# Performance work log

Hardware: AMD Instinct MI355X
Metric: run time of the kernel (lower is better)

Reference implementation:

```python
import jax, jax.numpy as jnp
import numpy as np

DIM = 1024
HID = 2048
E = 8
K = 2
INV_SQRT2 = 1.0 / 1.41421356237


def setup_inputs() -> dict:
    key = jax.random.key(0)
    ks = jax.random.split(key, 10)
    s = lambda fan_in: 1.0 / np.sqrt(fan_in)
    return {
        "x": jax.random.normal(ks[0], (4, 2048, DIM), dtype=jnp.float32),
        "gate_w": jax.random.uniform(ks[1], (DIM, E), jnp.float32, -s(DIM), s(DIM)),
        "gate_b": jnp.zeros((E,), jnp.float32),
        "w1": jax.random.uniform(ks[2], (E, DIM, HID), jnp.float32, -s(DIM), s(DIM)),
        "b1": jnp.zeros((E, HID), jnp.float32),
        "w2": jax.random.uniform(ks[3], (E, DIM, HID), jnp.float32, -s(DIM), s(DIM)),
        "b2": jnp.zeros((E, HID), jnp.float32),
        "w3": jax.random.uniform(ks[4], (E, HID, DIM), jnp.float32, -s(HID), s(HID)),
        "b3": jnp.zeros((E, DIM), jnp.float32),
    }


def reference(x, gate_w, gate_b, w1, b1, w2, b2, w3, b3):
    # Gating
    logits = jnp.einsum("bsd,de->bse", x, gate_w) + gate_b          # [b,s,E]
    scores = jax.nn.softmax(logits, axis=-1)
    topk_scores, topk_idx = jax.lax.top_k(scores, K)                  # [b,s,K]

    # Load-balance (entropy) loss over mean expert usage
    usage = scores.mean(axis=(0, 1))                                   # [E]
    lb_loss = -(usage * jnp.log(usage + 1e-9)).sum()

    # Per-token combine weight for each expert: score if expert in top-k else 0
    onehot = jax.nn.one_hot(topk_idx, E, dtype=x.dtype)               # [b,s,K,E]
    comb = (topk_scores[..., None] * onehot).sum(axis=2)              # [b,s,E]

    # SwiGLU experts (batched over E via einsum)
    h = jnp.einsum("bsd,edh->ebsh", x, w1) + b1[:, None, None, :]
    g = jax.nn.silu(jnp.einsum("bsd,edh->ebsh", x, w2) + b2[:, None, None, :])
    eo = jnp.einsum("ebsh,ehd->ebsd", h * g, w3) + b3[:, None, None, :]
    eo = eo * INV_SQRT2

    # Weighted combine (zero weight where expert not selected)
    out = jnp.einsum("ebsd,bse->bsd", eo, comb)
    return out, lb_loss
```

## Files before the change

kernel.cpp:

```cpp
#include <hip/hip_runtime.h>
#include <cstdio>

#define NTOK 8192
#define DIM 1024
#define HID 2048
#define NE 8
#define NPAIR (NTOK * 2)

typedef __attribute__((ext_vector_type(8))) short bf16x8;
typedef __attribute__((ext_vector_type(4))) float f32x4;

typedef const __attribute__((address_space(1))) void* gas_ptr;
typedef __attribute__((address_space(3))) void* las_ptr;

__device__ __forceinline__ void async16(const void* g, void* s) {
  __builtin_amdgcn_global_load_lds((gas_ptr)g, (las_ptr)s, 16, 0, 0);
}

__device__ __forceinline__ unsigned short f2bf(float f) {
  unsigned int u = __float_as_uint(f);
  u = (u + 0x7fff + ((u >> 16) & 1)) >> 16;
  return (unsigned short)u;
}

__device__ __forceinline__ float bf2f(unsigned short u) {
  return __uint_as_float((unsigned int)u << 16);
}


#define S_BARRIER __builtin_amdgcn_s_barrier()
#define VM_WAIT(N) asm volatile("s_waitcnt vmcnt(" #N ")" ::: "memory")
#define LGKM0 asm volatile("s_waitcnt lgkmcnt(0)" ::: "memory")
#define CFENCE asm volatile("" ::: "memory")

__global__ __launch_bounds__(256) void prep_kernel(
    const float* __restrict__ w1, const float* __restrict__ w2,
    const float* __restrict__ w3, unsigned short* __restrict__ w1bt,
    unsigned short* __restrict__ w2bt, unsigned short* __restrict__ w3bt) {
  const int z = blockIdx.y;
  const int m = z >> 3, e = z & 7;
  int R, C;
  const float* in;
  unsigned short* outp;
  if (m == 0)      { R = DIM; C = HID; in = w1; outp = w1bt; }
  else if (m == 1) { R = DIM; C = HID; in = w2; outp = w2bt; }
  else             { R = HID; C = DIM; in = w3; outp = w3bt; }
  in += (size_t)e * DIM * HID;
  outp += (size_t)e * DIM * HID;

  const int tilesx = C >> 6;
  const int c0 = (blockIdx.x % tilesx) * 64;
  const int r0 = (blockIdx.x / tilesx) * 64;

  __shared__ float tT[64][65];
  const int tid = threadIdx.x;
  const int cq = tid & 15;
  const int rr = tid >> 4;

#pragma unroll
  for (int p = 0; p < 4; p++) {
    const int r = rr + p * 16;
    const float4 v = *(const float4*)(in + (size_t)(r0 + r) * C + c0 + cq * 4);
    tT[cq * 4 + 0][r] = v.x;
    tT[cq * 4 + 1][r] = v.y;
    tT[cq * 4 + 2][r] = v.z;
    tT[cq * 4 + 3][r] = v.w;
  }
  __syncthreads();
#pragma unroll
  for (int p = 0; p < 4; p++) {
    const int cc = rr + p * 16;
    ushort4 o;
    o.x = f2bf(tT[cc][cq * 4 + 0]);
    o.y = f2bf(tT[cc][cq * 4 + 1]);
    o.z = f2bf(tT[cc][cq * 4 + 2]);
    o.w = f2bf(tT[cc][cq * 4 + 3]);
    *(ushort4*)(outp + (size_t)(c0 + cc) * R + r0 + cq * 4) = o;
  }
}

__global__ __launch_bounds__(256) void gate_kernel(
    const float* __restrict__ x, const float* __restrict__ gw,
    const float* __restrict__ gb, unsigned short* __restrict__ xb,
    float* __restrict__ scores, int* __restrict__ route_e,
    float* __restrict__ route_w) {
  __shared__ float sgwT[NE][DIM];
  const int tid = threadIdx.x;
#pragma unroll
  for (int i = 0; i < 8; i++) {
    const int j = i * 256 + tid;
    const float4 v = ((const float4*)gw)[j];
    const int d = j >> 1, e0 = (j & 1) * 4;
    sgwT[e0 + 0][d] = v.x; sgwT[e0 + 1][d] = v.y;
    sgwT[e0 + 2][d] = v.z; sgwT[e0 + 3][d] = v.w;
  }
  __syncthreads();

  const int wv = tid >> 6, lane = tid & 63;
  const int t = blockIdx.x * 4 + wv;
  float acc[NE] = {0.f, 0.f, 0.f, 0.f, 0.f, 0.f, 0.f, 0.f};
  const float4* x4 = (const float4*)(x + (size_t)t * DIM);
#pragma unroll
  for (int i = 0; i < 4; i++) {
    const float4 xv = x4[i * 64 + lane];
    const int d4 = i * 64 + lane;
    ushort4 xbv;
    xbv.x = f2bf(xv.x); xbv.y = f2bf(xv.y);
    xbv.z = f2bf(xv.z); xbv.w = f2bf(xv.w);
    *(ushort4*)(xb + (size_t)t * DIM + d4 * 4) = xbv;
#pragma unroll
    for (int e = 0; e < NE; e++) {
      const float4 wv4 = *(const float4*)&sgwT[e][d4 * 4];
      acc[e] += xv.x * wv4.x + xv.y * wv4.y + xv.z * wv4.z + xv.w * wv4.w;
    }
  }
#pragma unroll
  for (int e = 0; e < NE; e++)
#pragma unroll
    for (int s = 32; s; s >>= 1) acc[e] += __shfl_xor(acc[e], s, 64);

  if (lane == 0) {
    float l[NE], m = -1e30f;
#pragma unroll
    for (int e = 0; e < NE; e++) { l[e] = acc[e] + gb[e]; m = fmaxf(m, l[e]); }
    float p[NE], sum = 0.f;
#pragma unroll
    for (int e = 0; e < NE; e++) { p[e] = __expf(l[e] - m); sum += p[e]; }
    const float inv = 1.f / sum;
    float s[NE];
#pragma unroll
    for (int e = 0; e < NE; e++) { s[e] = p[e] * inv; scores[t * NE + e] = s[e]; }
    int i1 = 0;
    for (int e = 1; e < NE; e++) if (s[e] > s[i1]) i1 = e;
    int i2 = -1;
    for (int e = 0; e < NE; e++) {
      if (e == i1) continue;
      if (i2 < 0 || s[e] > s[i2]) i2 = e;
    }
    route_e[t * 2] = i1; route_e[t * 2 + 1] = i2;
    route_w[t * 2] = s[i1]; route_w[t * 2 + 1] = s[i2];
  }
}

__global__ void finalize_kernel(const float* __restrict__ scores,
                                const int* __restrict__ route_e,
                                int* __restrict__ ctrl,
                                float* __restrict__ out_lb) {
  __shared__ float red[1024];
  __shared__ int hist[NE];
  const int tid = threadIdx.x;
  if (tid < NE) hist[tid] = 0;
  const int e = tid & 7, row = tid >> 3;
  float s = 0.f;
  for (int i = 0; i < 64; i++) s += scores[(size_t)(row + i * 128) * NE + e];
  red[tid] = s;
  __syncthreads();
#pragma unroll
  for (int i = 0; i < 16; i++)
    atomicAdd(&hist[route_e[i * 1024 + tid]], 1);
  for (int st = 512; st >= 8; st >>= 1) {
    __syncthreads();
    if (tid < st) red[tid] += red[tid + st];
  }
  __syncthreads();
  if (tid == 0) {
    float lb = 0.f;
    for (int ee = 0; ee < NE; ee++) {
      const float u = red[ee] * (1.f / 8192.f);
      lb -= u * __logf(u + 1e-9f);
    }
    *out_lb = lb;
    int o = 0;
    for (int ee = 0; ee < NE; ee++) {
      ctrl[ee] = hist[ee];
      ctrl[8 + ee] = o;
      ctrl[17 + ee] = o;
      o += hist[ee];
    }
    ctrl[16] = o;
  }
}

__global__ __launch_bounds__(256) void scatter_kernel(
    const int* __restrict__ route_e, const float* __restrict__ route_w,
    int* __restrict__ ctrl, int* __restrict__ tok_list,
    float* __restrict__ pair_w, int* __restrict__ pair_pos) {
  __shared__ int lh[NE];
  __shared__ int lbase[NE];
  const int tid = threadIdx.x;
  const int t = blockIdx.x * 256 + tid;
  if (tid < NE) lh[tid] = 0;
  __syncthreads();
  const int e0 = route_e[t * 2], e1 = route_e[t * 2 + 1];
  const int p0 = atomicAdd(&lh[e0], 1);
  const int p1 = atomicAdd(&lh[e1], 1);
  __syncthreads();
  if (tid < NE) lbase[tid] = atomicAdd(&ctrl[17 + tid], lh[tid]);
  __syncthreads();
  const int q0 = lbase[e0] + p0;
  const int q1 = lbase[e1] + p1;
  tok_list[q0] = t;
  pair_w[q0] = route_w[t * 2] * 0.70710678118654752f;
  pair_pos[t * 2] = q0;
  tok_list[q1] = t;
  pair_w[q1] = route_w[t * 2 + 1] * 0.70710678118654752f;
  pair_pos[t * 2 + 1] = q1;
}

__global__ __launch_bounds__(512) void stage1_kernel(
    const unsigned short* __restrict__ xb, const unsigned short* __restrict__ w1bt,
    const unsigned short* __restrict__ w2bt, const float* __restrict__ b1,
    const float* __restrict__ b2, const int* __restrict__ tok_list,
    const int* __restrict__ ctrl, unsigned short* __restrict__ act) {
  const int hbid = blockIdx.x;
  const int lid = ((hbid & 7) << 9) + (hbid >> 3);
  const int e = lid >> 9;
  const int ytile = (lid >> 4) & 31;
  const int h0 = (lid & 15) * 128;

  const int cnt = ctrl[e];
  if (ytile * 256 >= cnt) return;
  const int off = ctrl[8 + e];
  const int rows = min(256, cnt - ytile * 256);

  __shared__ unsigned short sX[4][256 * 32];
  __shared__ unsigned short sW1[4][128 * 32];
  __shared__ unsigned short sW2[4][128 * 32];

  const int tid = threadIdx.x;
  const int wv = tid >> 6, lane = tid & 63;

  const int cl = ((tid & 3) ^ ((tid >> 3) & 3)) * 8;

  const unsigned short* w1p = w1bt + (size_t)e * HID * DIM + (size_t)h0 * DIM;
  const unsigned short* w2p = w2bt + (size_t)e * HID * DIM + (size_t)h0 * DIM;
  const unsigned short* gx0 =
      xb + (size_t)tok_list[off + ytile * 256 + min(tid >> 2, rows - 1)] * DIM + cl;
  const unsigned short* gx1 =
      xb + (size_t)tok_list[off + ytile * 256 + min(128 + (tid >> 2), rows - 1)] * DIM + cl;
  const unsigned short* gw1 = w1p + (size_t)(tid >> 2) * DIM + cl;
  const unsigned short* gw2 = w2p + (size_t)(tid >> 2) * DIM + cl;

  f32x4 ah[8][2], ag[8][2];
#pragma unroll
  for (int i = 0; i < 8; i++)
#pragma unroll
    for (int j = 0; j < 2; j++) {
      ah[i][j] = (f32x4){0.f, 0.f, 0.f, 0.f};
      ag[i][j] = (f32x4){0.f, 0.f, 0.f, 0.f};
    }

  const int wr = wv >> 2, wc = wv & 3;
  const int l15 = lane & 15, q = lane >> 4;
  const int pch = (q ^ ((l15 >> 1) & 3)) * 8;

#define S1_STAGE(B)                                   \
  do {                                                \
    async16(gx0, sX[B] + (wv * 64) * 8);              \
    async16(gx1, sX[B] + (512 + wv * 64) * 8);        \
    async16(gw1, sW1[B] + (wv * 64) * 8);             \
    async16(gw2, sW2[B] + (wv * 64) * 8);             \
    gx0 += 32; gx1 += 32; gw1 += 32; gw2 += 32;       \
  } while (0)

  S1_STAGE(0); S1_STAGE(1); S1_STAGE(2);
  VM_WAIT(8);
  S_BARRIER;
  CFENCE;

  const int NT = DIM / 32;
  for (int t = 0; t < NT; t++) {
    const int cur = t & 3;
    bf16x8 bx[8], a1[2], a2[2];
    {
      const unsigned short* xs = sX[cur];
      const unsigned short* w1s = sW1[cur];
      const unsigned short* w2s = sW2[cur];
#pragma unroll
      for (int i = 0; i < 8; i++)
        bx[i] = *(const bf16x8*)(xs + (wr * 128 + i * 16 + l15) * 32 + pch);
#pragma unroll
      for (int j = 0; j < 2; j++) {
        a1[j] = *(const bf16x8*)(w1s + (wc * 32 + j * 16 + l15) * 32 + pch);
        a2[j] = *(const bf16x8*)(w2s + (wc * 32 + j * 16 + l15) * 32 + pch);
      }
    }
    if (t < NT - 3) {
      const int nb = (t + 3) & 3;
      S1_STAGE(nb);
    }
    S_BARRIER;
    LGKM0;
    __builtin_amdgcn_sched_barrier(0);
    __builtin_amdgcn_s_setprio(1);
#pragma unroll
    for (int i = 0; i < 8; i++) {
      ah[i][0] = __builtin_amdgcn_mfma_f32_16x16x32_bf16(a1[0], bx[i], ah[i][0], 0, 0, 0);
      ag[i][0] = __builtin_amdgcn_mfma_f32_16x16x32_bf16(a2[0], bx[i], ag[i][0], 0, 0, 0);
      ah[i][1] = __builtin_amdgcn_mfma_f32_16x16x32_bf16(a1[1], bx[i], ah[i][1], 0, 0, 0);
      ag[i][1] = __builtin_amdgcn_mfma_f32_16x16x32_bf16(a2[1], bx[i], ag[i][1], 0, 0, 0);
    }
    __builtin_amdgcn_s_setprio(0);
    if (t < NT - 3) VM_WAIT(8);
    else if (t == NT - 3) VM_WAIT(4);
    else if (t == NT - 2) VM_WAIT(0);
    CFENCE;
    S_BARRIER;
  }
#undef S1_STAGE

  f32x4 b1v[2], b2v[2];
#pragma unroll
  for (int j = 0; j < 2; j++) {
    const int hc = h0 + wc * 32 + j * 16 + q * 4;
    b1v[j] = *(const f32x4*)(b1 + e * HID + hc);
    b2v[j] = *(const f32x4*)(b2 + e * HID + hc);
  }
#pragma unroll
  for (int i = 0; i < 8; i++) {
    const int trow = wr * 128 + i * 16 + l15;
    if (trow < rows) {
      const size_t gp = (size_t)(off + ytile * 256 + trow) * HID;
#pragma unroll
      for (int j = 0; j < 2; j++) {
        const int hc = h0 + wc * 32 + j * 16 + q * 4;
        ushort4 o;
        {
          const float hh = ah[i][j][0] + b1v[j][0];
          const float gg = ag[i][j][0] + b2v[j][0];
          o.x = f2bf(hh * (gg / (1.f + __expf(-gg))));
        }
        {
          const float hh = ah[i][j][1] + b1v[j][1];
          const float gg = ag[i][j][1] + b2v[j][1];
          o.y = f2bf(hh * (gg / (1.f + __expf(-gg))));
        }
        {
          const float hh = ah[i][j][2] + b1v[j][2];
          const float gg = ag[i][j][2] + b2v[j][2];
          o.z = f2bf(hh * (gg / (1.f + __expf(-gg))));
        }
        {
          const float hh = ah[i][j][3] + b1v[j][3];
          const float gg = ag[i][j][3] + b2v[j][3];
          o.w = f2bf(hh * (gg / (1.f + __expf(-gg))));
        }
        *(ushort4*)(act + gp + hc) = o;
      }
    }
  }
}

__global__ __launch_bounds__(512) void stage2s_kernel(
    const unsigned short* __restrict__ act, const unsigned short* __restrict__ w3bt,
    const float* __restrict__ b3, const float* __restrict__ pair_w,
    const int* __restrict__ ctrl, unsigned short* __restrict__ pair_out) {
  const int hbid = blockIdx.x;
  const int lid = ((hbid & 7) << 7) + (hbid >> 3);
  const int e = lid >> 7;
  const int ytile = (lid >> 2) & 31;
  const int d0 = (lid & 3) * 256;

  const int cnt = ctrl[e];
  if (ytile * 256 >= cnt) return;
  const int off = ctrl[8 + e];
  const int rows = min(256, cnt - ytile * 256);
  const int rbase = off + ytile * 256;

  __shared__ unsigned short sA[4][256 * 32];
  __shared__ unsigned short sW[4][256 * 32];

  const int tid = threadIdx.x;
  const int wv = tid >> 6, lane = tid & 63;
  const int cl = ((tid & 3) ^ ((tid >> 3) & 3)) * 8;

  const unsigned short* w3p = w3bt + (size_t)e * DIM * HID + (size_t)d0 * HID;
  const unsigned short* ga0 =
      act + (size_t)(rbase + min(tid >> 2, rows - 1)) * HID + cl;
  const unsigned short* ga1 =
      act + (size_t)(rbase + min(128 + (tid >> 2), rows - 1)) * HID + cl;
  const unsigned short* gw0 = w3p + (size_t)(tid >> 2) * HID + cl;
  const unsigned short* gw1 = w3p + (size_t)(128 + (tid >> 2)) * HID + cl;

  f32x4 acc[8][4];
#pragma unroll
  for (int i = 0; i < 8; i++)
#pragma unroll
    for (int j = 0; j < 4; j++) acc[i][j] = (f32x4){0.f, 0.f, 0.f, 0.f};

  const int wr = wv >> 2, wc = wv & 3;
  const int l15 = lane & 15, q = lane >> 4;
  const int pch = (q ^ ((l15 >> 1) & 3)) * 8;

#define S2_STAGE(B)                                   \
  do {                                                \
    async16(ga0, sA[B] + (wv * 64) * 8);              \
    async16(ga1, sA[B] + (512 + wv * 64) * 8);        \
    async16(gw0, sW[B] + (wv * 64) * 8);              \
    async16(gw1, sW[B] + (512 + wv * 64) * 8);        \
    ga0 += 32; ga1 += 32; gw0 += 32; gw1 += 32;       \
  } while (0)

  S2_STAGE(0); S2_STAGE(1); S2_STAGE(2);
  VM_WAIT(8);
  S_BARRIER;
  CFENCE;

  const int NT = HID / 32;
  for (int t = 0; t < NT; t++) {
    const int cur = t & 3;
    bf16x8 af[8], bf[4];
    {
      const unsigned short* as = sA[cur];
      const unsigned short* ws = sW[cur];
#pragma unroll
      for (int i = 0; i < 8; i++)
        af[i] = *(const bf16x8*)(as + (wr * 128 + i * 16 + l15) * 32 + pch);
#pragma unroll
      for (int j = 0; j < 4; j++)
        bf[j] = *(const bf16x8*)(ws + (wc * 64 + j * 16 + l15) * 32 + pch);
    }
    if (t < NT - 3) {
      const int nb = (t + 3) & 3;
      S2_STAGE(nb);
    }
    S_BARRIER;
    LGKM0;
    __builtin_amdgcn_sched_barrier(0);
    __builtin_amdgcn_s_setprio(1);
#pragma unroll
    for (int i = 0; i < 8; i++)
#pragma unroll
      for (int j = 0; j < 4; j++)
        acc[i][j] =
            __builtin_amdgcn_mfma_f32_16x16x32_bf16(af[i], bf[j], acc[i][j], 0, 0, 0);
    __builtin_amdgcn_s_setprio(0);
    if (t < NT - 3) VM_WAIT(8);
    else if (t == NT - 3) VM_WAIT(4);
    else if (t == NT - 2) VM_WAIT(0);
    CFENCE;
    S_BARRIER;
  }
#undef S2_STAGE

#pragma unroll
  for (int i = 0; i < 8; i++)
#pragma unroll
    for (int rg = 0; rg < 4; rg++) {
      const int row = wr * 128 + i * 16 + q * 4 + rg;
      if (row < rows) {
        const int pr = rbase + row;
        const float wt = pair_w[pr];
#pragma unroll
        for (int j = 0; j < 4; j++) {
          const int dcol = d0 + wc * 64 + j * 16 + l15;
          pair_out[(size_t)pr * DIM + dcol] = f2bf((acc[i][j][rg] + b3[e * DIM + dcol]) * wt);
        }
      }
    }
}

__global__ __launch_bounds__(512) void stage2a_kernel(
    const unsigned short* __restrict__ act, const unsigned short* __restrict__ w3bt,
    const float* __restrict__ b3, const int* __restrict__ tok_list,
    const float* __restrict__ pair_w, const int* __restrict__ ctrl,
    float* __restrict__ out) {
  const int hbid = blockIdx.x;
  const int lid = ((hbid & 7) << 7) + (hbid >> 3);
  const int e = lid >> 7;
  const int ytile = (lid >> 2) & 31;
  const int d0 = (lid & 3) * 256;

  const int cnt = ctrl[e];
  if (ytile * 256 >= cnt) return;
  const int off = ctrl[8 + e];
  const int rows = min(256, cnt - ytile * 256);
  const int rbase = off + ytile * 256;

  __shared__ unsigned short sA[4][256 * 32];
  __shared__ unsigned short sW[4][256 * 32];

  const int tid = threadIdx.x;
  const int wv = tid >> 6, lane = tid & 63;
  const int cl = ((tid & 3) ^ ((tid >> 3) & 3)) * 8;

  const unsigned short* w3p = w3bt + (size_t)e * DIM * HID + (size_t)d0 * HID;
  const unsigned short* ga0 =
      act + (size_t)(rbase + min(tid >> 2, rows - 1)) * HID + cl;
  const unsigned short* ga1 =
      act + (size_t)(rbase + min(128 + (tid >> 2), rows - 1)) * HID + cl;
  const unsigned short* gw0 = w3p + (size_t)(tid >> 2) * HID + cl;
  const unsigned short* gw1 = w3p + (size_t)(128 + (tid >> 2)) * HID + cl;

  f32x4 acc[8][4];
#pragma unroll
  for (int i = 0; i < 8; i++)
#pragma unroll
    for (int j = 0; j < 4; j++) acc[i][j] = (f32x4){0.f, 0.f, 0.f, 0.f};

  const int wr = wv >> 2, wc = wv & 3;
  const int l15 = lane & 15, q = lane >> 4;
  const int pch = (q ^ ((l15 >> 1) & 3)) * 8;

#define S2A_STAGE(B)                                  \
  do {                                                \
    async16(ga0, sA[B] + (wv * 64) * 8);              \
    async16(ga1, sA[B] + (512 + wv * 64) * 8);        \
    async16(gw0, sW[B] + (wv * 64) * 8);              \
    async16(gw1, sW[B] + (512 + wv * 64) * 8);        \
    ga0 += 32; ga1 += 32; gw0 += 32; gw1 += 32;       \
  } while (0)

  S2A_STAGE(0); S2A_STAGE(1); S2A_STAGE(2);
  VM_WAIT(8);
  S_BARRIER;
  CFENCE;

  const int NT = HID / 32;
  for (int t = 0; t < NT; t++) {
    const int cur = t & 3;
    bf16x8 af[8], bf[4];
    {
      const unsigned short* as = sA[cur];
      const unsigned short* ws = sW[cur];
#pragma unroll
      for (int i = 0; i < 8; i++)
        af[i] = *(const bf16x8*)(as + (wr * 128 + i * 16 + l15) * 32 + pch);
#pragma unroll
      for (int j = 0; j < 4; j++)
        bf[j] = *(const bf16x8*)(ws + (wc * 64 + j * 16 + l15) * 32 + pch);
    }
    if (t < NT - 3) {
      const int nb = (t + 3) & 3;
      S2A_STAGE(nb);
    }
    S_BARRIER;
    LGKM0;
    __builtin_amdgcn_sched_barrier(0);
    __builtin_amdgcn_s_setprio(1);
#pragma unroll
    for (int i = 0; i < 8; i++)
#pragma unroll
      for (int j = 0; j < 4; j++)
        acc[i][j] =
            __builtin_amdgcn_mfma_f32_16x16x32_bf16(af[i], bf[j], acc[i][j], 0, 0, 0);
    __builtin_amdgcn_s_setprio(0);
    if (t < NT - 3) VM_WAIT(8);
    else if (t == NT - 3) VM_WAIT(4);
    else if (t == NT - 2) VM_WAIT(0);
    CFENCE;
    S_BARRIER;
  }
#undef S2A_STAGE

#pragma unroll
  for (int i = 0; i < 8; i++)
#pragma unroll
    for (int rg = 0; rg < 4; rg++) {
      const int row = wr * 128 + i * 16 + q * 4 + rg;
      if (row < rows) {
        const int pr = rbase + row;
        const int tok = tok_list[pr];
        const float wt = pair_w[pr];
#pragma unroll
        for (int j = 0; j < 4; j++) {
          const int dcol = d0 + wc * 64 + j * 16 + l15;
          atomicAdd(out + (size_t)tok * DIM + dcol, (acc[i][j][rg] + b3[e * DIM + dcol]) * wt);
        }
      }
    }
}

__global__ __launch_bounds__(256) void combine_kernel(
    const unsigned short* __restrict__ pair_out, const int* __restrict__ pair_pos,
    float* __restrict__ out) {
  const int t = blockIdx.x;
  const int d = threadIdx.x * 4;
  const int p0 = pair_pos[t * 2], p1 = pair_pos[t * 2 + 1];
  const ushort4 a = *(const ushort4*)(pair_out + (size_t)p0 * DIM + d);
  const ushort4 b = *(const ushort4*)(pair_out + (size_t)p1 * DIM + d);
  float4 r;
  r.x = bf2f(a.x) + bf2f(b.x);
  r.y = bf2f(a.y) + bf2f(b.y);
  r.z = bf2f(a.z) + bf2f(b.z);
  r.w = bf2f(a.w) + bf2f(b.w);
  *(float4*)(out + (size_t)t * DIM + d) = r;
}

static const size_t SZ_XB  = (size_t)NTOK * DIM * 2;
static const size_t SZ_W   = (size_t)NE * DIM * HID * 2;
static const size_t SZ_ACT = (size_t)NPAIR * HID * 2;
static const size_t OFF_XB  = 0;
static const size_t OFF_W1  = OFF_XB + SZ_XB;
static const size_t OFF_W2  = OFF_W1 + SZ_W;
static const size_t OFF_W3  = OFF_W2 + SZ_W;
static const size_t OFF_ACT = OFF_W3 + SZ_W;
static const size_t OFF_SC  = OFF_ACT + SZ_ACT;
static const size_t OFF_RE  = OFF_SC + (size_t)NTOK * NE * 4;
static const size_t OFF_RW  = OFF_RE + (size_t)NPAIR * 4;
static const size_t OFF_TL  = OFF_RW + (size_t)NPAIR * 4;
static const size_t OFF_PW  = OFF_TL + (size_t)NPAIR * 4;
static const size_t OFF_PP  = OFF_PW + (size_t)NPAIR * 4;
static const size_t OFF_CT  = OFF_PP + (size_t)NPAIR * 4;
static const size_t WS_BASE = OFF_CT + 128;
static const size_t OFF_PO  = WS_BASE;
static const size_t WS_FULL = OFF_PO + (size_t)NPAIR * DIM * 2;

extern "C" void kernel_launch(void* const* d_in, const int* in_sizes, int n_in,
                              void* d_out, int out_size, void* d_ws, size_t ws_size,
                              hipStream_t stream) {
  const float* x      = (const float*)d_in[0];
  const float* gate_w = (const float*)d_in[1];
  const float* gate_b = (const float*)d_in[2];
  const float* w1     = (const float*)d_in[3];
  const float* b1     = (const float*)d_in[4];
  const float* w2     = (const float*)d_in[5];
  const float* b2     = (const float*)d_in[6];
  const float* w3     = (const float*)d_in[7];
  const float* b3     = (const float*)d_in[8];
  float* out = (float*)d_out;

  if (ws_size < WS_BASE) {
    fprintf(stderr, "kernel_launch: ws_size %zu < needed %zu\n", ws_size, WS_BASE);
    return;
  }
  const bool store_path = (ws_size >= WS_FULL);

  char* ws = (char*)d_ws;
  unsigned short* xb   = (unsigned short*)(ws + OFF_XB);
  unsigned short* w1bt = (unsigned short*)(ws + OFF_W1);
  unsigned short* w2bt = (unsigned short*)(ws + OFF_W2);
  unsigned short* w3bt = (unsigned short*)(ws + OFF_W3);
  unsigned short* act  = (unsigned short*)(ws + OFF_ACT);
  float* scores        = (float*)(ws + OFF_SC);
  int* route_e         = (int*)(ws + OFF_RE);
  float* route_w       = (float*)(ws + OFF_RW);
  int* tok_list        = (int*)(ws + OFF_TL);
  float* pair_w        = (float*)(ws + OFF_PW);
  int* pair_pos        = (int*)(ws + OFF_PP);
  int* ctrl            = (int*)(ws + OFF_CT);
  unsigned short* pout = (unsigned short*)(ws + OFF_PO);

  if (!store_path)
    hipMemsetAsync(d_out, 0, (size_t)out_size * sizeof(float), stream);

  prep_kernel<<<dim3(512, 24), 256, 0, stream>>>(w1, w2, w3, w1bt, w2bt, w3bt);
  gate_kernel<<<2048, 256, 0, stream>>>(x, gate_w, gate_b, xb, scores, route_e,
                                        route_w);
  finalize_kernel<<<1, 1024, 0, stream>>>(scores, route_e, ctrl, out + (out_size - 1));
  scatter_kernel<<<32, 256, 0, stream>>>(route_e, route_w, ctrl, tok_list, pair_w,
                                         pair_pos);
  stage1_kernel<<<4096, 512, 0, stream>>>(xb, w1bt, w2bt, b1, b2, tok_list, ctrl, act);
  if (store_path) {
    stage2s_kernel<<<1024, 512, 0, stream>>>(act, w3bt, b3, pair_w, ctrl, pout);
    combine_kernel<<<NTOK, 256, 0, stream>>>(pout, pair_pos, out);
  } else {
    stage2a_kernel<<<1024, 512, 0, stream>>>(act, w3bt, b3, tok_list, pair_w,
                                             ctrl, out);
  }
}
```

Before: 568.0 us.

## Drop mid-loop barrier in GEMM pipelines and fuse weight-prep with gating launch

```diff
diff --git a/kernel.cpp b/kernel.cpp
--- a/kernel.cpp
+++ b/kernel.cpp
@@ -33,59 +33,63 @@
 #define LGKM0 asm volatile("s_waitcnt lgkmcnt(0)" ::: "memory")
 #define CFENCE asm volatile("" ::: "memory")
 
-__global__ __launch_bounds__(256) void prep_kernel(
+__global__ __launch_bounds__(256) void prepgate_kernel(
     const float* __restrict__ w1, const float* __restrict__ w2,
     const float* __restrict__ w3, unsigned short* __restrict__ w1bt,
-    unsigned short* __restrict__ w2bt, unsigned short* __restrict__ w3bt) {
-  const int z = blockIdx.y;
-  const int m = z >> 3, e = z & 7;
-  int R, C;
-  const float* in;
-  unsigned short* outp;
-  if (m == 0)      { R = DIM; C = HID; in = w1; outp = w1bt; }
-  else if (m == 1) { R = DIM; C = HID; in = w2; outp = w2bt; }
-  else             { R = HID; C = DIM; in = w3; outp = w3bt; }
-  in += (size_t)e * DIM * HID;
-  outp += (size_t)e * DIM * HID;
-
-  const int tilesx = C >> 6;
-  const int c0 = (blockIdx.x % tilesx) * 64;
-  const int r0 = (blockIdx.x / tilesx) * 64;
-
-  __shared__ float tT[64][65];
-  const int tid = threadIdx.x;
-  const int cq = tid & 15;
-  const int rr = tid >> 4;
-
-#pragma unroll
-  for (int p = 0; p < 4; p++) {
-    const int r = rr + p * 16;
-    const float4 v = *(const float4*)(in + (size_t)(r0 + r) * C + c0 + cq * 4);
-    tT[cq * 4 + 0][r] = v.x;
-    tT[cq * 4 + 1][r] = v.y;
-    tT[cq * 4 + 2][r] = v.z;
-    tT[cq * 4 + 3][r] = v.w;
-  }
-  __syncthreads();
-#pragma unroll
-  for (int p = 0; p < 4; p++) {
-    const int cc = rr + p * 16;
-    ushort4 o;
-    o.x = f2bf(tT[cc][cq * 4 + 0]);
-    o.y = f2bf(tT[cc][cq * 4 + 1]);
-    o.z = f2bf(tT[cc][cq * 4 + 2]);
-    o.w = f2bf(tT[cc][cq * 4 + 3]);
-    *(ushort4*)(outp + (size_t)(c0 + cc) * R + r0 + cq * 4) = o;
-  }
-}
-
-__global__ __launch_bounds__(256) void gate_kernel(
+    unsigned short* __restrict__ w2bt, unsigned short* __restrict__ w3bt,
     const float* __restrict__ x, const float* __restrict__ gw,
     const float* __restrict__ gb, unsigned short* __restrict__ xb,
     float* __restrict__ scores, int* __restrict__ route_e,
     float* __restrict__ route_w) {
-  __shared__ float sgwT[NE][DIM];
+  __shared__ float smem[NE * DIM];
+  const int bx = blockIdx.x;
   const int tid = threadIdx.x;
+
+  if (bx < 12288) {
+    float (*tT)[65] = reinterpret_cast<float(*)[65]>(smem);
+    const int z = bx >> 9;
+    const int bxx = bx & 511;
+    const int m = z >> 3, e = z & 7;
+    int R, C;
+    const float* in;
+    unsigned short* outp;
+    if (m == 0)      { R = DIM; C = HID; in = w1; outp = w1bt; }
+    else if (m == 1) { R = DIM; C = HID; in = w2; outp = w2bt; }
+    else             { R = HID; C = DIM; in = w3; outp = w3bt; }
+    in += (size_t)e * DIM * HID;
+    outp += (size_t)e * DIM * HID;
+
+    const int tilesx = C >> 6;
+    const int c0 = (bxx % tilesx) * 64;
+    const int r0 = (bxx / tilesx) * 64;
+
+    const int cq = tid & 15;
+    const int rr = tid >> 4;
+#pragma unroll
+    for (int p = 0; p < 4; p++) {
+      const int r = rr + p * 16;
+      const float4 v = *(const float4*)(in + (size_t)(r0 + r) * C + c0 + cq * 4);
+      tT[cq * 4 + 0][r] = v.x;
+      tT[cq * 4 + 1][r] = v.y;
+      tT[cq * 4 + 2][r] = v.z;
+      tT[cq * 4 + 3][r] = v.w;
+    }
+    __syncthreads();
+#pragma unroll
+    for (int p = 0; p < 4; p++) {
+      const int cc = rr + p * 16;
+      ushort4 o;
+      o.x = f2bf(tT[cc][cq * 4 + 0]);
+      o.y = f2bf(tT[cc][cq * 4 + 1]);
+      o.z = f2bf(tT[cc][cq * 4 + 2]);
+      o.w = f2bf(tT[cc][cq * 4 + 3]);
+      *(ushort4*)(outp + (size_t)(c0 + cc) * R + r0 + cq * 4) = o;
+    }
+    return;
+  }
+
+  float (*sgwT)[DIM] = reinterpret_cast<float(*)[DIM]>(smem);
+  const int g = bx - 12288;
 #pragma unroll
   for (int i = 0; i < 8; i++) {
     const int j = i * 256 + tid;
@@ -97,7 +101,7 @@
   __syncthreads();
 
   const int wv = tid >> 6, lane = tid & 63;
-  const int t = blockIdx.x * 4 + wv;
+  const int t = g * 4 + wv;
   float acc[NE] = {0.f, 0.f, 0.f, 0.f, 0.f, 0.f, 0.f, 0.f};
   const float4* x4 = (const float4*)(x + (size_t)t * DIM);
 #pragma unroll
@@ -229,7 +233,6 @@
 
   const int tid = threadIdx.x;
   const int wv = tid >> 6, lane = tid & 63;
-
   const int cl = ((tid & 3) ^ ((tid >> 3) & 3)) * 8;
 
   const unsigned short* w1p = w1bt + (size_t)e * HID * DIM + (size_t)h0 * DIM;
@@ -277,21 +280,18 @@
       const unsigned short* w1s = sW1[cur];
       const unsigned short* w2s = sW2[cur];
 #pragma unroll
-      for (int i = 0; i < 8; i++)
-        bx[i] = *(const bf16x8*)(xs + (wr * 128 + i * 16 + l15) * 32 + pch);
-#pragma unroll
       for (int j = 0; j < 2; j++) {
         a1[j] = *(const bf16x8*)(w1s + (wc * 32 + j * 16 + l15) * 32 + pch);
         a2[j] = *(const bf16x8*)(w2s + (wc * 32 + j * 16 + l15) * 32 + pch);
       }
+#pragma unroll
+      for (int i = 0; i < 8; i++)
+        bx[i] = *(const bf16x8*)(xs + (wr * 128 + i * 16 + l15) * 32 + pch);
     }
     if (t < NT - 3) {
       const int nb = (t + 3) & 3;
       S1_STAGE(nb);
     }
-    S_BARRIER;
-    LGKM0;
-    __builtin_amdgcn_sched_barrier(0);
     __builtin_amdgcn_s_setprio(1);
 #pragma unroll
     for (int i = 0; i < 8; i++) {
@@ -301,6 +301,8 @@
       ag[i][1] = __builtin_amdgcn_mfma_f32_16x16x32_bf16(a2[1], bx[i], ag[i][1], 0, 0, 0);
     }
     __builtin_amdgcn_s_setprio(0);
+    LGKM0;
+    __builtin_amdgcn_sched_barrier(0);
     if (t < NT - 3) VM_WAIT(8);
     else if (t == NT - 3) VM_WAIT(4);
     else if (t == NT - 2) VM_WAIT(0);
@@ -414,19 +416,16 @@
       const unsigned short* as = sA[cur];
       const unsigned short* ws = sW[cur];
 #pragma unroll
+      for (int j = 0; j < 4; j++)
+        bf[j] = *(const bf16x8*)(ws + (wc * 64 + j * 16 + l15) * 32 + pch);
+#pragma unroll
       for (int i = 0; i < 8; i++)
         af[i] = *(const bf16x8*)(as + (wr * 128 + i * 16 + l15) * 32 + pch);
-#pragma unroll
-      for (int j = 0; j < 4; j++)
-        bf[j] = *(const bf16x8*)(ws + (wc * 64 + j * 16 + l15) * 32 + pch);
     }
     if (t < NT - 3) {
       const int nb = (t + 3) & 3;
       S2_STAGE(nb);
     }
-    S_BARRIER;
-    LGKM0;
-    __builtin_amdgcn_sched_barrier(0);
     __builtin_amdgcn_s_setprio(1);
 #pragma unroll
     for (int i = 0; i < 8; i++)
@@ -435,6 +434,8 @@
         acc[i][j] =
             __builtin_amdgcn_mfma_f32_16x16x32_bf16(af[i], bf[j], acc[i][j], 0, 0, 0);
     __builtin_amdgcn_s_setprio(0);
+    LGKM0;
+    __builtin_amdgcn_sched_barrier(0);
     if (t < NT - 3) VM_WAIT(8);
     else if (t == NT - 3) VM_WAIT(4);
     else if (t == NT - 2) VM_WAIT(0);
@@ -524,19 +525,16 @@
       const unsigned short* as = sA[cur];
       const unsigned short* ws = sW[cur];
 #pragma unroll
+      for (int j = 0; j < 4; j++)
+        bf[j] = *(const bf16x8*)(ws + (wc * 64 + j * 16 + l15) * 32 + pch);
+#pragma unroll
       for (int i = 0; i < 8; i++)
         af[i] = *(const bf16x8*)(as + (wr * 128 + i * 16 + l15) * 32 + pch);
-#pragma unroll
-      for (int j = 0; j < 4; j++)
-        bf[j] = *(const bf16x8*)(ws + (wc * 64 + j * 16 + l15) * 32 + pch);
     }
     if (t < NT - 3) {
       const int nb = (t + 3) & 3;
       S2A_STAGE(nb);
     }
-    S_BARRIER;
-    LGKM0;
-    __builtin_amdgcn_sched_barrier(0);
     __builtin_amdgcn_s_setprio(1);
 #pragma unroll
     for (int i = 0; i < 8; i++)
@@ -545,6 +543,8 @@
         acc[i][j] =
             __builtin_amdgcn_mfma_f32_16x16x32_bf16(af[i], bf[j], acc[i][j], 0, 0, 0);
     __builtin_amdgcn_s_setprio(0);
+    LGKM0;
+    __builtin_amdgcn_sched_barrier(0);
     if (t < NT - 3) VM_WAIT(8);
     else if (t == NT - 3) VM_WAIT(4);
     else if (t == NT - 2) VM_WAIT(0);
@@ -644,9 +644,9 @@
   if (!store_path)
     hipMemsetAsync(d_out, 0, (size_t)out_size * sizeof(float), stream);
 
-  prep_kernel<<<dim3(512, 24), 256, 0, stream>>>(w1, w2, w3, w1bt, w2bt, w3bt);
-  gate_kernel<<<2048, 256, 0, stream>>>(x, gate_w, gate_b, xb, scores, route_e,
-                                        route_w);
+  prepgate_kernel<<<14336, 256, 0, stream>>>(w1, w2, w3, w1bt, w2bt, w3bt,
+                                             x, gate_w, gate_b, xb, scores,
+                                             route_e, route_w);
   finalize_kernel<<<1, 1024, 0, stream>>>(scores, route_e, ctrl, out + (out_size - 1));
   scatter_kernel<<<32, 256, 0, stream>>>(route_e, route_w, ctrl, tok_list, pair_w,
                                          pair_pos);
```

New measurement: 544.0 us. 1.04x faster.
